# Kernel optimization log

Hardware: AMD Instinct MI355X
Metric: run time of the kernel (lower is better)

Reference implementation:

```python
import jax, jax.numpy as jnp
import numpy as np
import math

IN_DIM = 2048
OUT_DIM = 2048
BATCH = 4096
BN_EPS = 1e-5


def setup_inputs() -> dict:
    key = jax.random.key(0)
    ks = jax.random.split(key, 6)
    x = jax.random.normal(ks[0], (BATCH, IN_DIM), dtype=jnp.float32)
    # scale ~ N(1.0, 0.1), translate = 0
    scale = 1.0 + 0.1 * jax.random.normal(ks[1], (1, IN_DIM), dtype=jnp.float32)
    translate = jnp.zeros((1, IN_DIM), dtype=jnp.float32)
    # kaiming-normal-ish init for wave_weight (fan_in), orthogonal-ish for base_weight
    wave_weight = jax.random.normal(ks[2], (OUT_DIM, IN_DIM), dtype=jnp.float32) * np.sqrt(2.0 / IN_DIM)
    bw = jax.random.normal(ks[3], (OUT_DIM, IN_DIM), dtype=jnp.float32)
    q, _ = jnp.linalg.qr(bw.T)  # (IN_DIM, OUT_DIM) orthonormal columns
    base_weight = q.T.astype(jnp.float32)
    gamma = jnp.ones((OUT_DIM,), dtype=jnp.float32)
    beta = jnp.zeros((OUT_DIM,), dtype=jnp.float32)
    return {"x": x, "scale": scale, "translate": translate,
            "wave_weight": wave_weight, "base_weight": base_weight,
            "gamma": gamma, "beta": beta}


def reference(x, scale, translate, wave_weight, base_weight, gamma, beta):
    # Bio wavelet: pi^-1/4 * cos(3u) * exp(-0.5 u^2), u = (x - t) / clamp(s, 1e-3)
    u = (x - translate) / jnp.maximum(scale, 1e-3)            # (B, in)
    wavelet = (math.pi ** -0.25) * jnp.cos(3.0 * u) * jnp.exp(-0.5 * u * u)
    # einsum 'boi,oi->bo' with singleton o broadcast == plain matmul
    wave_out = jnp.einsum('bi,oi->bo', wavelet, wave_weight)  # (B, out)
    base_out = jnp.einsum('bi,oi->bo', x, base_weight)        # (B, out)
    y = wave_out + 0.3 * base_out
    # BatchNorm1d (training mode: batch statistics, biased variance)
    mean = jnp.mean(y, axis=0)
    var = jnp.mean(jnp.square(y - mean), axis=0)
    out = gamma * (y - mean) * jax.lax.rsqrt(var + BN_EPS) + beta
    # dropout treated as identity (deterministic reference)
    return out
```

## Files before the change

kernel.cpp:

```cpp
#include <hip/hip_runtime.h>
#include <stdint.h>

#define IN_DIM 2048
#define OUT_DIM 2048
#define BATCH 4096
#define KDIM (2 * IN_DIM)
#define KROWB (KDIM * 2)
#define BN_EPS 1e-5f

typedef __attribute__((ext_vector_type(8))) short bf16x8;
typedef __attribute__((ext_vector_type(4))) float f32x4;

__device__ __forceinline__ unsigned short f2bf(float f) {
  union { float f; unsigned u; } v; v.f = f;
  unsigned r = v.u + 0x7FFFu + ((v.u >> 16) & 1u);
  return (unsigned short)(r >> 16);
}

__global__ void prep_act(const float* __restrict__ x,
                         const float* __restrict__ scale,
                         const float* __restrict__ translate,
                         unsigned short* __restrict__ A) {
  int e = (blockIdx.x * 256 + threadIdx.x) * 4;
  int b = e / IN_DIM;
  int i = e % IN_DIM;
  float4 xv = *(const float4*)(x + e);
  float4 sv = *(const float4*)(scale + i);
  float4 tv = *(const float4*)(translate + i);
  const float c = 0.7511255444649425f;
  float u0 = (xv.x - tv.x) / fmaxf(sv.x, 1e-3f);
  float u1 = (xv.y - tv.y) / fmaxf(sv.y, 1e-3f);
  float u2 = (xv.z - tv.z) / fmaxf(sv.z, 1e-3f);
  float u3 = (xv.w - tv.w) / fmaxf(sv.w, 1e-3f);
  ushort4 wv, xb;
  wv.x = f2bf(c * __cosf(3.0f * u0) * __expf(-0.5f * u0 * u0));
  wv.y = f2bf(c * __cosf(3.0f * u1) * __expf(-0.5f * u1 * u1));
  wv.z = f2bf(c * __cosf(3.0f * u2) * __expf(-0.5f * u2 * u2));
  wv.w = f2bf(c * __cosf(3.0f * u3) * __expf(-0.5f * u3 * u3));
  xb.x = f2bf(xv.x); xb.y = f2bf(xv.y); xb.z = f2bf(xv.z); xb.w = f2bf(xv.w);
  *(ushort4*)(A + (size_t)b * KDIM + i) = wv;
  *(ushort4*)(A + (size_t)b * KDIM + IN_DIM + i) = xb;
}

__global__ void prep_w(const float* __restrict__ ww,
                       const float* __restrict__ bw,
                       unsigned short* __restrict__ W) {
  int e = (blockIdx.x * 256 + threadIdx.x) * 4;
  int o = e / IN_DIM;
  int k = e % IN_DIM;
  float4 a = *(const float4*)(ww + e);
  float4 b = *(const float4*)(bw + e);
  ushort4 wa, wb;
  wa.x = f2bf(a.x); wa.y = f2bf(a.y); wa.z = f2bf(a.z); wa.w = f2bf(a.w);
  wb.x = f2bf(0.3f * b.x); wb.y = f2bf(0.3f * b.y);
  wb.z = f2bf(0.3f * b.z); wb.w = f2bf(0.3f * b.w);
  *(ushort4*)(W + (size_t)o * KDIM + k) = wa;
  *(ushort4*)(W + (size_t)o * KDIM + IN_DIM + k) = wb;
}


#define GLDS(gp, lo) __builtin_amdgcn_global_load_lds( \
    (const __attribute__((address_space(1))) void*)(gp), \
    (__attribute__((address_space(3))) void*)(lds + (lo) + ldsw), 16, 0, 0)

#define MM32() do { \
  __builtin_amdgcn_s_setprio(1); \
  _Pragma("unroll") for (int i2 = 0; i2 < 4; ++i2) \
  _Pragma("unroll") for (int j2 = 0; j2 < 8; ++j2) \
    acc[i2][j2] = __builtin_amdgcn_mfma_f32_16x16x32_bf16( \
        af[i2], bq[j2], acc[i2][j2], 0, 0, 0); \
  __builtin_amdgcn_s_setprio(0); \
} while (0)

#define LGKM0() asm volatile("s_waitcnt lgkmcnt(0)" ::: "memory")
#define VMW8()  asm volatile("s_waitcnt vmcnt(8)" ::: "memory")
#define VMW0()  asm volatile("s_waitcnt vmcnt(0)" ::: "memory")
#define NOW()   do { } while (0)
#define BAR()   do { asm volatile("" ::: "memory"); __builtin_amdgcn_s_barrier(); \
                     asm volatile("" ::: "memory"); } while (0)

#define KT(S, SS, TOFS, DOST, TAILW) do { \
  const char* Lr = lds + (S) * 16384; \
  af[0] = *(const bf16x8*)(Lr + aoff + 0 * 1024 + roff); \
  af[1] = *(const bf16x8*)(Lr + aoff + 1 * 1024 + roff); \
  af[2] = *(const bf16x8*)(Lr + aoff + 2 * 1024 + roff); \
  af[3] = *(const bf16x8*)(Lr + aoff + 3 * 1024 + roff); \
  bq[0] = *(const bf16x8*)(Lr + 8192 + 0 * 1024 + roff); \
  bq[1] = *(const bf16x8*)(Lr + 8192 + 1 * 1024 + roff); \
  bq[2] = *(const bf16x8*)(Lr + 8192 + 2 * 1024 + roff); \
  bq[3] = *(const bf16x8*)(Lr + 8192 + 3 * 1024 + roff); \
  bq[4] = *(const bf16x8*)(Lr + 8192 + 4 * 1024 + roff); \
  bq[5] = *(const bf16x8*)(Lr + 8192 + 5 * 1024 + roff); \
  bq[6] = *(const bf16x8*)(Lr + 8192 + 6 * 1024 + roff); \
  bq[7] = *(const bf16x8*)(Lr + 8192 + 7 * 1024 + roff); \
  if (DOST) { \
    GLDS(aG + (TOFS),              (SS) * 16384 + 0); \
    GLDS(aG + (TOFS) + 32 * KROWB, (SS) * 16384 + 2048); \
    GLDS(aG + (TOFS) + 64 * KROWB, (SS) * 16384 + 4096); \
    GLDS(aG + (TOFS) + 96 * KROWB, (SS) * 16384 + 6144); \
    GLDS(bG + (TOFS),              (SS) * 16384 + 8192); \
    GLDS(bG + (TOFS) + 32 * KROWB, (SS) * 16384 + 10240); \
    GLDS(bG + (TOFS) + 64 * KROWB, (SS) * 16384 + 12288); \
    GLDS(bG + (TOFS) + 96 * KROWB, (SS) * 16384 + 14336); \
  } \
  MM32(); \
  LGKM0(); TAILW; BAR(); \
} while (0)

__global__ __launch_bounds__(128, 1) void gemm128(
    const unsigned short* __restrict__ A,
    const unsigned short* __restrict__ W,
    float* __restrict__ Y,
    float* __restrict__ sums, float* __restrict__ sqs) {
  __shared__ char lds[49152];
  const int tid = threadIdx.x;
  const int lane = tid & 63;
  const int w = tid >> 6;

  const int xcd = blockIdx.x & 7;
  const int li = blockIdx.x >> 3;
  const int bcol = (xcd * 2 + (li >> 5)) * 128;
  const int brow = (li & 31) * 128;

  const int srow2 = 2 * (tid >> 3) + ((tid >> 2) & 1);
  const int sksl = (tid & 3) ^ ((tid >> 3) & 3);
  const char* aG = (const char*)A + (size_t)(brow + srow2) * KROWB + sksl * 16;
  const char* bG = (const char*)W + (size_t)(bcol + srow2) * KROWB + sksl * 16;
  const int ldsw = w * 1024;

  const int lh = (lane & 15) >> 1;
  const int roff = lh * 128 + (lane & 1) * 64 + (((lane >> 4) ^ (lh & 3)) << 4);
  const int aoff = w * 4096;

  f32x4 acc[4][8];
#pragma unroll
  for (int m = 0; m < 4; ++m)
#pragma unroll
    for (int n = 0; n < 8; ++n)
      acc[m][n] = (f32x4){0.f, 0.f, 0.f, 0.f};
  bf16x8 af[4], bq[8];

  GLDS(aG, 0); GLDS(aG + 32 * KROWB, 2048);
  GLDS(aG + 64 * KROWB, 4096); GLDS(aG + 96 * KROWB, 6144);
  GLDS(bG, 8192); GLDS(bG + 32 * KROWB, 10240);
  GLDS(bG + 64 * KROWB, 12288); GLDS(bG + 96 * KROWB, 14336);
  GLDS(aG + 64, 16384); GLDS(aG + 32 * KROWB + 64, 16384 + 2048);
  GLDS(aG + 64 * KROWB + 64, 16384 + 4096); GLDS(aG + 96 * KROWB + 64, 16384 + 6144);
  GLDS(bG + 64, 16384 + 8192); GLDS(bG + 32 * KROWB + 64, 16384 + 10240);
  GLDS(bG + 64 * KROWB + 64, 16384 + 12288); GLDS(bG + 96 * KROWB + 64, 16384 + 14336);
  VMW8(); BAR();

  for (int tt = 0; tt < 123; tt += 3) {
    KT(0, 2, (tt + 2) * 64, 1, VMW8());
    KT(1, 0, (tt + 3) * 64, 1, VMW8());
    KT(2, 1, (tt + 4) * 64, 1, VMW8());
  }
  KT(0, 2, 125 * 64, 1, VMW8());
  KT(1, 0, 126 * 64, 1, VMW8());
  KT(2, 1, 127 * 64, 1, VMW8());
  KT(0, 0, 0, 0, VMW0());
  KT(1, 0, 0, 0, NOW());

  const int r0 = brow + w * 64 + (lane >> 4) * 4;
  const int c0 = bcol + (lane & 15);
#pragma unroll
  for (int m = 0; m < 4; ++m)
#pragma unroll
    for (int n = 0; n < 8; ++n)
#pragma unroll
      for (int j = 0; j < 4; ++j)
        Y[(size_t)(r0 + m * 16 + j) * OUT_DIM + (c0 + n * 16)] = acc[m][n][j];

#pragma unroll
  for (int n = 0; n < 8; ++n) {
    float s = 0.f, q = 0.f;
#pragma unroll
    for (int m = 0; m < 4; ++m)
#pragma unroll
      for (int j = 0; j < 4; ++j) {
        float v = acc[m][n][j];
        s += v; q += v * v;
      }
    s += __shfl_xor(s, 16); q += __shfl_xor(q, 16);
    s += __shfl_xor(s, 32); q += __shfl_xor(q, 32);
    if (lane < 16) {
      atomicAdd(&sums[c0 + n * 16], s);
      atomicAdd(&sqs[c0 + n * 16], q);
    }
  }
}

__global__ void bnorm(float* __restrict__ Y,
                      const float* __restrict__ sums, const float* __restrict__ sqs,
                      const float* __restrict__ gamma, const float* __restrict__ beta) {
  int e = (blockIdx.x * 256 + threadIdx.x) * 4;
  int c = e % OUT_DIM;
  float4 y = *(float4*)(Y + e);
  float4 s = *(const float4*)(sums + c);
  float4 q = *(const float4*)(sqs + c);
  float4 g = *(const float4*)(gamma + c);
  float4 bb = *(const float4*)(beta + c);
  const float invB = 1.0f / (float)BATCH;
  float m0 = s.x * invB, m1 = s.y * invB, m2 = s.z * invB, m3 = s.w * invB;
  float i0 = rsqrtf(q.x * invB - m0 * m0 + BN_EPS);
  float i1 = rsqrtf(q.y * invB - m1 * m1 + BN_EPS);
  float i2 = rsqrtf(q.z * invB - m2 * m2 + BN_EPS);
  float i3 = rsqrtf(q.w * invB - m3 * m3 + BN_EPS);
  y.x = g.x * (y.x - m0) * i0 + bb.x;
  y.y = g.y * (y.y - m1) * i1 + bb.y;
  y.z = g.z * (y.z - m2) * i2 + bb.z;
  y.w = g.w * (y.w - m3) * i3 + bb.w;
  *(float4*)(Y + e) = y;
}

extern "C" void kernel_launch(void* const* d_in, const int* in_sizes, int n_in,
                              void* d_out, int out_size, void* d_ws, size_t ws_size,
                              hipStream_t stream) {
  const float* x         = (const float*)d_in[0];
  const float* scale     = (const float*)d_in[1];
  const float* translate = (const float*)d_in[2];
  const float* ww        = (const float*)d_in[3];
  const float* bw        = (const float*)d_in[4];
  const float* gamma     = (const float*)d_in[5];
  const float* beta      = (const float*)d_in[6];
  float* out = (float*)d_out;

  char* ws = (char*)d_ws;
  unsigned short* A = (unsigned short*)ws;
  unsigned short* W = (unsigned short*)(ws + 33554432);
  float* sums = (float*)(ws + 50331648);
  float* sqs  = sums + OUT_DIM;

  hipMemsetAsync(sums, 0, 2 * OUT_DIM * sizeof(float), stream);
  prep_act<<<(BATCH * IN_DIM) / 1024, 256, 0, stream>>>(x, scale, translate, A);
  prep_w<<<(OUT_DIM * IN_DIM) / 1024, 256, 0, stream>>>(ww, bw, W);
  gemm128<<<512, 128, 0, stream>>>(A, W, out, sums, sqs);
  bnorm<<<(BATCH * OUT_DIM) / 1024, 256, 0, stream>>>(out, sums, sqs, gamma, beta);
}
```

Measured before the change: 120.2 us.

## Use 4-wave GEMM blocks with 4-stage LDS pipeline and merge prep kernels

The GEMM moves from 2 waves per 128x128 tile to 4 waves in a 2x2 arrangement, so each wave holds a 64x64 accumulator instead of 64x128. The LDS ring buffer grows from three to four stages with matching waitcnt accounting. LDS fragment loads now come after the global-to-LDS prefetch is issued. Separately, the two bf16 prep kernels are merged into one launch to save a launch and a gap. The aim is more waves per CU to hide latency and lower register pressure, at the cost of more LDS per block and more LDS read traffic per MFMA.

```diff
diff --git a/kernel.cpp b/kernel.cpp
--- a/kernel.cpp
+++ b/kernel.cpp
@@ -17,45 +17,46 @@
   return (unsigned short)(r >> 16);
 }
 
-__global__ void prep_act(const float* __restrict__ x,
+__global__ void prep_all(const float* __restrict__ x,
                          const float* __restrict__ scale,
                          const float* __restrict__ translate,
-                         unsigned short* __restrict__ A) {
-  int e = (blockIdx.x * 256 + threadIdx.x) * 4;
-  int b = e / IN_DIM;
-  int i = e % IN_DIM;
-  float4 xv = *(const float4*)(x + e);
-  float4 sv = *(const float4*)(scale + i);
-  float4 tv = *(const float4*)(translate + i);
-  const float c = 0.7511255444649425f;
-  float u0 = (xv.x - tv.x) / fmaxf(sv.x, 1e-3f);
-  float u1 = (xv.y - tv.y) / fmaxf(sv.y, 1e-3f);
-  float u2 = (xv.z - tv.z) / fmaxf(sv.z, 1e-3f);
-  float u3 = (xv.w - tv.w) / fmaxf(sv.w, 1e-3f);
-  ushort4 wv, xb;
-  wv.x = f2bf(c * __cosf(3.0f * u0) * __expf(-0.5f * u0 * u0));
-  wv.y = f2bf(c * __cosf(3.0f * u1) * __expf(-0.5f * u1 * u1));
-  wv.z = f2bf(c * __cosf(3.0f * u2) * __expf(-0.5f * u2 * u2));
-  wv.w = f2bf(c * __cosf(3.0f * u3) * __expf(-0.5f * u3 * u3));
-  xb.x = f2bf(xv.x); xb.y = f2bf(xv.y); xb.z = f2bf(xv.z); xb.w = f2bf(xv.w);
-  *(ushort4*)(A + (size_t)b * KDIM + i) = wv;
-  *(ushort4*)(A + (size_t)b * KDIM + IN_DIM + i) = xb;
-}
-
-__global__ void prep_w(const float* __restrict__ ww,
-                       const float* __restrict__ bw,
-                       unsigned short* __restrict__ W) {
-  int e = (blockIdx.x * 256 + threadIdx.x) * 4;
-  int o = e / IN_DIM;
-  int k = e % IN_DIM;
-  float4 a = *(const float4*)(ww + e);
-  float4 b = *(const float4*)(bw + e);
-  ushort4 wa, wb;
-  wa.x = f2bf(a.x); wa.y = f2bf(a.y); wa.z = f2bf(a.z); wa.w = f2bf(a.w);
-  wb.x = f2bf(0.3f * b.x); wb.y = f2bf(0.3f * b.y);
-  wb.z = f2bf(0.3f * b.z); wb.w = f2bf(0.3f * b.w);
-  *(ushort4*)(W + (size_t)o * KDIM + k) = wa;
-  *(ushort4*)(W + (size_t)o * KDIM + IN_DIM + k) = wb;
+                         const float* __restrict__ ww,
+                         const float* __restrict__ bw,
+                         unsigned short* __restrict__ A,
+                         unsigned short* __restrict__ W) {
+  if (blockIdx.x < 8192) {
+    int e = (blockIdx.x * 256 + threadIdx.x) * 4;
+    int b = e / IN_DIM;
+    int i = e % IN_DIM;
+    float4 xv = *(const float4*)(x + e);
+    float4 sv = *(const float4*)(scale + i);
+    float4 tv = *(const float4*)(translate + i);
+    const float c = 0.7511255444649425f;
+    float u0 = (xv.x - tv.x) / fmaxf(sv.x, 1e-3f);
+    float u1 = (xv.y - tv.y) / fmaxf(sv.y, 1e-3f);
+    float u2 = (xv.z - tv.z) / fmaxf(sv.z, 1e-3f);
+    float u3 = (xv.w - tv.w) / fmaxf(sv.w, 1e-3f);
+    ushort4 wv, xb;
+    wv.x = f2bf(c * __cosf(3.0f * u0) * __expf(-0.5f * u0 * u0));
+    wv.y = f2bf(c * __cosf(3.0f * u1) * __expf(-0.5f * u1 * u1));
+    wv.z = f2bf(c * __cosf(3.0f * u2) * __expf(-0.5f * u2 * u2));
+    wv.w = f2bf(c * __cosf(3.0f * u3) * __expf(-0.5f * u3 * u3));
+    xb.x = f2bf(xv.x); xb.y = f2bf(xv.y); xb.z = f2bf(xv.z); xb.w = f2bf(xv.w);
+    *(ushort4*)(A + (size_t)b * KDIM + i) = wv;
+    *(ushort4*)(A + (size_t)b * KDIM + IN_DIM + i) = xb;
+  } else {
+    int e = ((blockIdx.x - 8192) * 256 + threadIdx.x) * 4;
+    int o = e / IN_DIM;
+    int k = e % IN_DIM;
+    float4 a = *(const float4*)(ww + e);
+    float4 b = *(const float4*)(bw + e);
+    ushort4 wa, wb;
+    wa.x = f2bf(a.x); wa.y = f2bf(a.y); wa.z = f2bf(a.z); wa.w = f2bf(a.w);
+    wb.x = f2bf(0.3f * b.x); wb.y = f2bf(0.3f * b.y);
+    wb.z = f2bf(0.3f * b.z); wb.w = f2bf(0.3f * b.w);
+    *(ushort4*)(W + (size_t)o * KDIM + k) = wa;
+    *(ushort4*)(W + (size_t)o * KDIM + IN_DIM + k) = wb;
+  }
 }
 
 
@@ -63,59 +64,55 @@
     (const __attribute__((address_space(1))) void*)(gp), \
     (__attribute__((address_space(3))) void*)(lds + (lo) + ldsw), 16, 0, 0)
 
-#define MM32() do { \
+#define MM16() do { \
   __builtin_amdgcn_s_setprio(1); \
   _Pragma("unroll") for (int i2 = 0; i2 < 4; ++i2) \
-  _Pragma("unroll") for (int j2 = 0; j2 < 8; ++j2) \
+  _Pragma("unroll") for (int j2 = 0; j2 < 4; ++j2) \
     acc[i2][j2] = __builtin_amdgcn_mfma_f32_16x16x32_bf16( \
         af[i2], bq[j2], acc[i2][j2], 0, 0, 0); \
   __builtin_amdgcn_s_setprio(0); \
 } while (0)
 
-#define LGKM0() asm volatile("s_waitcnt lgkmcnt(0)" ::: "memory")
-#define VMW8()  asm volatile("s_waitcnt vmcnt(8)" ::: "memory")
-#define VMW0()  asm volatile("s_waitcnt vmcnt(0)" ::: "memory")
-#define NOW()   do { } while (0)
+#define WAIT_V8L0() asm volatile("s_waitcnt vmcnt(8) lgkmcnt(0)" ::: "memory")
+#define WAIT_V4L0() asm volatile("s_waitcnt vmcnt(4) lgkmcnt(0)" ::: "memory")
+#define WAIT_V0L0() asm volatile("s_waitcnt vmcnt(0) lgkmcnt(0)" ::: "memory")
+#define WAIT_L0()   asm volatile("s_waitcnt lgkmcnt(0)" ::: "memory")
 #define BAR()   do { asm volatile("" ::: "memory"); __builtin_amdgcn_s_barrier(); \
                      asm volatile("" ::: "memory"); } while (0)
 
 #define KT(S, SS, TOFS, DOST, TAILW) do { \
-  const char* Lr = lds + (S) * 16384; \
-  af[0] = *(const bf16x8*)(Lr + aoff + 0 * 1024 + roff); \
-  af[1] = *(const bf16x8*)(Lr + aoff + 1 * 1024 + roff); \
-  af[2] = *(const bf16x8*)(Lr + aoff + 2 * 1024 + roff); \
-  af[3] = *(const bf16x8*)(Lr + aoff + 3 * 1024 + roff); \
-  bq[0] = *(const bf16x8*)(Lr + 8192 + 0 * 1024 + roff); \
-  bq[1] = *(const bf16x8*)(Lr + 8192 + 1 * 1024 + roff); \
-  bq[2] = *(const bf16x8*)(Lr + 8192 + 2 * 1024 + roff); \
-  bq[3] = *(const bf16x8*)(Lr + 8192 + 3 * 1024 + roff); \
-  bq[4] = *(const bf16x8*)(Lr + 8192 + 4 * 1024 + roff); \
-  bq[5] = *(const bf16x8*)(Lr + 8192 + 5 * 1024 + roff); \
-  bq[6] = *(const bf16x8*)(Lr + 8192 + 6 * 1024 + roff); \
-  bq[7] = *(const bf16x8*)(Lr + 8192 + 7 * 1024 + roff); \
   if (DOST) { \
     GLDS(aG + (TOFS),              (SS) * 16384 + 0); \
-    GLDS(aG + (TOFS) + 32 * KROWB, (SS) * 16384 + 2048); \
     GLDS(aG + (TOFS) + 64 * KROWB, (SS) * 16384 + 4096); \
-    GLDS(aG + (TOFS) + 96 * KROWB, (SS) * 16384 + 6144); \
     GLDS(bG + (TOFS),              (SS) * 16384 + 8192); \
-    GLDS(bG + (TOFS) + 32 * KROWB, (SS) * 16384 + 10240); \
     GLDS(bG + (TOFS) + 64 * KROWB, (SS) * 16384 + 12288); \
-    GLDS(bG + (TOFS) + 96 * KROWB, (SS) * 16384 + 14336); \
   } \
-  MM32(); \
-  LGKM0(); TAILW; BAR(); \
+  { \
+    const char* Lr = lds + (S) * 16384; \
+    af[0] = *(const bf16x8*)(Lr + aoff + 0 * 1024 + roff); \
+    af[1] = *(const bf16x8*)(Lr + aoff + 1 * 1024 + roff); \
+    af[2] = *(const bf16x8*)(Lr + aoff + 2 * 1024 + roff); \
+    af[3] = *(const bf16x8*)(Lr + aoff + 3 * 1024 + roff); \
+    bq[0] = *(const bf16x8*)(Lr + boff + 0 * 1024 + roff); \
+    bq[1] = *(const bf16x8*)(Lr + boff + 1 * 1024 + roff); \
+    bq[2] = *(const bf16x8*)(Lr + boff + 2 * 1024 + roff); \
+    bq[3] = *(const bf16x8*)(Lr + boff + 3 * 1024 + roff); \
+    MM16(); \
+  } \
+  TAILW; BAR(); \
 } while (0)
 
-__global__ __launch_bounds__(128, 1) void gemm128(
+__global__ __launch_bounds__(256, 2) void gemm128q(
     const unsigned short* __restrict__ A,
     const unsigned short* __restrict__ W,
     float* __restrict__ Y,
     float* __restrict__ sums, float* __restrict__ sqs) {
-  __shared__ char lds[49152];
+  __shared__ char lds[65536];
   const int tid = threadIdx.x;
   const int lane = tid & 63;
-  const int w = tid >> 6;
+  const int wave = tid >> 6;
+  const int wr = wave >> 1;
+  const int wc = wave & 1;
 
   const int xcd = blockIdx.x & 7;
   const int li = blockIdx.x >> 3;
@@ -126,53 +123,52 @@
   const int sksl = (tid & 3) ^ ((tid >> 3) & 3);
   const char* aG = (const char*)A + (size_t)(brow + srow2) * KROWB + sksl * 16;
   const char* bG = (const char*)W + (size_t)(bcol + srow2) * KROWB + sksl * 16;
-  const int ldsw = w * 1024;
+  const int ldsw = wave * 1024;
 
   const int lh = (lane & 15) >> 1;
   const int roff = lh * 128 + (lane & 1) * 64 + (((lane >> 4) ^ (lh & 3)) << 4);
-  const int aoff = w * 4096;
-
-  f32x4 acc[4][8];
+  const int aoff = wr * 4096;
+  const int boff = 8192 + wc * 4096;
+
+  f32x4 acc[4][4];
 #pragma unroll
   for (int m = 0; m < 4; ++m)
 #pragma unroll
-    for (int n = 0; n < 8; ++n)
+    for (int n = 0; n < 4; ++n)
       acc[m][n] = (f32x4){0.f, 0.f, 0.f, 0.f};
-  bf16x8 af[4], bq[8];
-
-  GLDS(aG, 0); GLDS(aG + 32 * KROWB, 2048);
-  GLDS(aG + 64 * KROWB, 4096); GLDS(aG + 96 * KROWB, 6144);
-  GLDS(bG, 8192); GLDS(bG + 32 * KROWB, 10240);
-  GLDS(bG + 64 * KROWB, 12288); GLDS(bG + 96 * KROWB, 14336);
-  GLDS(aG + 64, 16384); GLDS(aG + 32 * KROWB + 64, 16384 + 2048);
-  GLDS(aG + 64 * KROWB + 64, 16384 + 4096); GLDS(aG + 96 * KROWB + 64, 16384 + 6144);
-  GLDS(bG + 64, 16384 + 8192); GLDS(bG + 32 * KROWB + 64, 16384 + 10240);
-  GLDS(bG + 64 * KROWB + 64, 16384 + 12288); GLDS(bG + 96 * KROWB + 64, 16384 + 14336);
-  VMW8(); BAR();
-
-  for (int tt = 0; tt < 123; tt += 3) {
-    KT(0, 2, (tt + 2) * 64, 1, VMW8());
-    KT(1, 0, (tt + 3) * 64, 1, VMW8());
-    KT(2, 1, (tt + 4) * 64, 1, VMW8());
+  bf16x8 af[4], bq[4];
+
+  GLDS(aG, 0); GLDS(aG + 64 * KROWB, 4096);
+  GLDS(bG, 8192); GLDS(bG + 64 * KROWB, 12288);
+  GLDS(aG + 64, 16384); GLDS(aG + 64 * KROWB + 64, 16384 + 4096);
+  GLDS(bG + 64, 16384 + 8192); GLDS(bG + 64 * KROWB + 64, 16384 + 12288);
+  GLDS(aG + 128, 32768); GLDS(aG + 64 * KROWB + 128, 32768 + 4096);
+  GLDS(bG + 128, 32768 + 8192); GLDS(bG + 64 * KROWB + 128, 32768 + 12288);
+  asm volatile("s_waitcnt vmcnt(8)" ::: "memory"); BAR();
+
+  for (int tt = 0; tt < 124; tt += 4) {
+    KT(0, 3, (tt + 3) * 64, 1, WAIT_V8L0());
+    KT(1, 0, (tt + 4) * 64, 1, WAIT_V8L0());
+    KT(2, 1, (tt + 5) * 64, 1, WAIT_V8L0());
+    KT(3, 2, (tt + 6) * 64, 1, WAIT_V8L0());
   }
-  KT(0, 2, 125 * 64, 1, VMW8());
-  KT(1, 0, 126 * 64, 1, VMW8());
-  KT(2, 1, 127 * 64, 1, VMW8());
-  KT(0, 0, 0, 0, VMW0());
-  KT(1, 0, 0, 0, NOW());
-
-  const int r0 = brow + w * 64 + (lane >> 4) * 4;
-  const int c0 = bcol + (lane & 15);
+  KT(0, 3, 127 * 64, 1, WAIT_V8L0());
+  KT(1, 0, 0, 0, WAIT_V4L0());
+  KT(2, 0, 0, 0, WAIT_V0L0());
+  KT(3, 0, 0, 0, WAIT_L0());
+
+  const int r0 = brow + wr * 64 + (lane >> 4) * 4;
+  const int c0 = bcol + wc * 64 + (lane & 15);
 #pragma unroll
   for (int m = 0; m < 4; ++m)
 #pragma unroll
-    for (int n = 0; n < 8; ++n)
+    for (int n = 0; n < 4; ++n)
 #pragma unroll
       for (int j = 0; j < 4; ++j)
         Y[(size_t)(r0 + m * 16 + j) * OUT_DIM + (c0 + n * 16)] = acc[m][n][j];
 
 #pragma unroll
-  for (int n = 0; n < 8; ++n) {
+  for (int n = 0; n < 4; ++n) {
     float s = 0.f, q = 0.f;
 #pragma unroll
     for (int m = 0; m < 4; ++m)
@@ -232,8 +228,7 @@
   float* sqs  = sums + OUT_DIM;
 
   hipMemsetAsync(sums, 0, 2 * OUT_DIM * sizeof(float), stream);
-  prep_act<<<(BATCH * IN_DIM) / 1024, 256, 0, stream>>>(x, scale, translate, A);
-  prep_w<<<(OUT_DIM * IN_DIM) / 1024, 256, 0, stream>>>(ww, bw, W);
-  gemm128<<<512, 128, 0, stream>>>(A, W, out, sums, sqs);
+  prep_all<<<12288, 256, 0, stream>>>(x, scale, translate, ww, bw, A, W);
+  gemm128q<<<512, 256, 0, stream>>>(A, W, out, sums, sqs);
   bnorm<<<(BATCH * OUT_DIM) / 1024, 256, 0, stream>>>(out, sums, sqs, gamma, beta);
 }
```

New measurement: 125.6 us. 1.05x slower.
